# Kernel optimization log

Measured on AMD Instinct MI355X. Metric: run time of the kernel, lower is better.

## Reference

```python
import jax, jax.numpy as jnp
import numpy as np

B, L, T, H = 8, 16, 1024, 256


def setup_inputs() -> dict:
    key = jax.random.key(0)
    k1, k2 = jax.random.split(key)
    h_blth = jax.random.normal(k1, (B, L, T, H), dtype=jnp.float32)
    # nn.Linear(H, 1): weight [1, H] -> store as [H]; bias [1]
    attn_w = jax.random.normal(k2, (H,), dtype=jnp.float32) / np.sqrt(H)
    attn_b = jnp.zeros((1,), dtype=jnp.float32)
    return {"h_blth": h_blth, "attn_w": attn_w, "attn_b": attn_b}


def reference(h_blth, attn_w, attn_b):
    # scores: [B, L, T]
    s = jnp.einsum('blth,h->blt', h_blth, attn_w) + attn_b[0]
    # global max over T (matches torch .max(dim=2, keepdim=True))
    s_max = jnp.max(s, axis=2, keepdims=True)
    exp_s = jnp.exp(s - s_max)                      # [B, L, T]
    cum_exp = jnp.cumsum(exp_s, axis=2)             # [B, L, T]
    weighted_h = exp_s[..., None] * h_blth          # [B, L, T, H]
    cum_weighted_h = jnp.cumsum(weighted_h, axis=2) # [B, L, T, H]
    ctx = cum_weighted_h / (cum_exp[..., None] + 1e-12)
    return h_blth + ctx
```

## Files before the change

### kernel.cpp

```cpp
#include <hip/hip_runtime.h>


constexpr int Tn = 1024, Hn = 256;
constexpr int BL = 128;
constexpr int NCH = 8;
constexpr int CT = Tn / NCH;
constexpr int F4 = Hn / 4;

__global__ __launch_bounds__(256) void k_scores(const float* __restrict__ h,
                                                const float* __restrict__ w,
                                                const float* __restrict__ bias,
                                                float* __restrict__ ebuf,
                                                float* __restrict__ P,
                                                float* __restrict__ Se) {
    const int wave = threadIdx.x >> 6, lane = threadIdx.x & 63;
    const int g = lane >> 4, sub = lane & 15;
    const int j = blockIdx.x & 7, bl = blockIdx.x >> 3;
    const float b0 = bias[0];
    const float4* wp = reinterpret_cast<const float4*>(w);
    float4 w4[4];
    #pragma unroll
    for (int q = 0; q < 4; ++q) w4[q] = wp[sub + 16 * q];
    const float4* hp = reinterpret_cast<const float4*>(h) + (size_t)bl * Tn * F4;
    const int t0 = j * CT + wave * 32;

    float4 acc[4] = {{0,0,0,0},{0,0,0,0},{0,0,0,0},{0,0,0,0}};
    float esum = 0.f;
    #pragma unroll
    for (int i = 0; i < 8; ++i) {
        const int t = t0 + i * 4 + g;
        float4 x[4];
        #pragma unroll
        for (int q = 0; q < 4; ++q) x[q] = hp[(size_t)t * F4 + sub + 16 * q];
        float p = 0.f;
        #pragma unroll
        for (int q = 0; q < 4; ++q) {
            p = fmaf(x[q].x, w4[q].x, p);
            p = fmaf(x[q].y, w4[q].y, p);
            p = fmaf(x[q].z, w4[q].z, p);
            p = fmaf(x[q].w, w4[q].w, p);
        }
        p += __shfl_xor(p, 1, 64);
        p += __shfl_xor(p, 2, 64);
        p += __shfl_xor(p, 4, 64);
        p += __shfl_xor(p, 8, 64);
        const float e = __expf(p + b0);
        esum += e;
        #pragma unroll
        for (int q = 0; q < 4; ++q) {
            acc[q].x = fmaf(e, x[q].x, acc[q].x);
            acc[q].y = fmaf(e, x[q].y, acc[q].y);
            acc[q].z = fmaf(e, x[q].z, acc[q].z);
            acc[q].w = fmaf(e, x[q].w, acc[q].w);
        }
        if (sub == 0) ebuf[bl * Tn + t] = e;
    }
    #pragma unroll
    for (int q = 0; q < 4; ++q) {
        acc[q].x += __shfl_xor(acc[q].x, 16, 64); acc[q].x += __shfl_xor(acc[q].x, 32, 64);
        acc[q].y += __shfl_xor(acc[q].y, 16, 64); acc[q].y += __shfl_xor(acc[q].y, 32, 64);
        acc[q].z += __shfl_xor(acc[q].z, 16, 64); acc[q].z += __shfl_xor(acc[q].z, 32, 64);
        acc[q].w += __shfl_xor(acc[q].w, 16, 64); acc[q].w += __shfl_xor(acc[q].w, 32, 64);
    }
    esum += __shfl_xor(esum, 16, 64);  esum += __shfl_xor(esum, 32, 64);

    __shared__ float4 redP[4][16][4];
    __shared__ float  redS[4];
    if (lane < 16) {
        #pragma unroll
        for (int q = 0; q < 4; ++q) redP[wave][lane][q] = acc[q];
    }
    if (lane == 0) redS[wave] = esum;
    __syncthreads();
    if (threadIdx.x < 64) {
        const int s16 = threadIdx.x & 15, q = threadIdx.x >> 4;
        float4 a = redP[0][s16][q], b = redP[1][s16][q];
        float4 c = redP[2][s16][q], d = redP[3][s16][q];
        float4 s;
        s.x = (a.x + b.x) + (c.x + d.x);
        s.y = (a.y + b.y) + (c.y + d.y);
        s.z = (a.z + b.z) + (c.z + d.z);
        s.w = (a.w + b.w) + (c.w + d.w);
        reinterpret_cast<float4*>(P)[(bl * NCH + j) * F4 + s16 + 16 * q] = s;
    } else if (threadIdx.x == 64) {
        Se[bl * NCH + j] = (redS[0] + redS[1]) + (redS[2] + redS[3]);
    }
}

__global__ __launch_bounds__(256) void k_apply(const float* __restrict__ h,
                                               const float* __restrict__ ebuf,
                                               const float* __restrict__ P,
                                               const float* __restrict__ Se,
                                               float* __restrict__ out) {
    const int j = blockIdx.x & 7, bl = blockIdx.x >> 3;
    const int tid = threadIdx.x;
    __shared__ float se[CT], sd[CT];
    if (tid < CT) se[tid] = ebuf[bl * Tn + j * CT + tid];
    __syncthreads();

    if (tid < 64) {
        float base = 0.f;
        for (int jj = 0; jj < j; ++jj) base += Se[bl * NCH + jj];
        float v0 = se[2 * tid], v1 = se[2 * tid + 1];
        float ts = v0 + v1;
        float sc = ts;
        #pragma unroll
        for (int off = 1; off < 64; off <<= 1) {
            float n = __shfl_up(sc, off, 64);
            if (tid >= off) sc += n;
        }
        float pre = base + sc - ts;
        float c0 = pre + v0, c1 = c0 + v1;
        sd[2 * tid]     = 1.0f / (c0 + 1e-12f);
        sd[2 * tid + 1] = 1.0f / (c1 + 1e-12f);
    }
    float acc = 0.f;
    for (int jj = 0; jj < j; ++jj) acc += P[(bl * NCH + jj) * Hn + tid];
    __syncthreads();

    const float* hp = h   + ((size_t)bl * Tn + j * CT) * Hn + tid;
    float*       op = out + ((size_t)bl * Tn + j * CT) * Hn + tid;

    for (int t = 0; t < CT; t += 16) {
        float x[16];
        #pragma unroll
        for (int u = 0; u < 16; ++u) x[u] = hp[(size_t)(t + u) * Hn];
        #pragma unroll
        for (int u = 0; u < 16; ++u) {
            acc = fmaf(se[t + u], x[u], acc);
            op[(size_t)(t + u) * Hn] = fmaf(acc, sd[t + u], x[u]);
        }
    }
}

extern "C" void kernel_launch(void* const* d_in, const int* in_sizes, int n_in,
                              void* d_out, int out_size, void* d_ws, size_t ws_size,
                              hipStream_t stream) {
    const float* h = (const float*)d_in[0];
    const float* w = (const float*)d_in[1];
    const float* b = (const float*)d_in[2];
    float* out = (float*)d_out;

    float* ebuf = (float*)d_ws;
    float* P    = ebuf + BL * Tn;
    float* Se   = P + BL * NCH * Hn;

    k_scores<<<BL * NCH, 256, 0, stream>>>(h, w, b, ebuf, P, Se);
    k_apply<<<BL * NCH, 256, 0, stream>>>(h, ebuf, P, Se, out);
}
```

Before: 253.8 us.

## Fuse score and apply kernels with decoupled-lookback chunk prefix and LDS-cached rows

Replaces the two-kernel design, where h was read twice from global memory, with a single kernel. Each block gets a dynamic ticket, loads a 64-row chunk into LDS, computes scores, exps and the chunk partial sums, and publishes them with a release flag. It then spin-waits on the flags of earlier chunks to build its prefix offset and writes the output from the LDS copy. This roughly halves the HBM reads of h, at the cost of a memset per call, serialized waits on predecessor chunks, and 64KB of LDS per block, which limits occupancy.

```diff
diff --git a/kernel.cpp b/kernel.cpp
--- a/kernel.cpp
+++ b/kernel.cpp
@@ -2,134 +2,124 @@
 
 
 constexpr int Tn = 1024, Hn = 256;
-constexpr int BL = 128;
-constexpr int NCH = 8;
-constexpr int CT = Tn / NCH;
-constexpr int F4 = Hn / 4;
+constexpr int BL   = 128;
+constexpr int CT   = 64;
+constexpr int NCH  = Tn / CT;
+constexpr int F4   = Hn / 4;
+constexpr int NBLK = BL * NCH;
 
-__global__ __launch_bounds__(256) void k_scores(const float* __restrict__ h,
-                                                const float* __restrict__ w,
-                                                const float* __restrict__ bias,
-                                                float* __restrict__ ebuf,
-                                                float* __restrict__ P,
-                                                float* __restrict__ Se) {
-    const int wave = threadIdx.x >> 6, lane = threadIdx.x & 63;
-    const int g = lane >> 4, sub = lane & 15;
-    const int j = blockIdx.x & 7, bl = blockIdx.x >> 3;
-    const float b0 = bias[0];
-    const float4* wp = reinterpret_cast<const float4*>(w);
-    float4 w4[4];
-    #pragma unroll
-    for (int q = 0; q < 4; ++q) w4[q] = wp[sub + 16 * q];
-    const float4* hp = reinterpret_cast<const float4*>(h) + (size_t)bl * Tn * F4;
-    const int t0 = j * CT + wave * 32;
+__global__ __launch_bounds__(256) void k_fused(
+    const float* __restrict__ h, const float* __restrict__ w,
+    const float* __restrict__ bias, float* __restrict__ out,
+    int* __restrict__ ticket, int* __restrict__ flags,
+    float* __restrict__ P, float* __restrict__ Se)
+{
+    const int tid  = threadIdx.x;
+    const int wv   = tid >> 6;
+    const int lane = tid & 63;
 
-    float4 acc[4] = {{0,0,0,0},{0,0,0,0},{0,0,0,0},{0,0,0,0}};
-    float esum = 0.f;
-    #pragma unroll
-    for (int i = 0; i < 8; ++i) {
-        const int t = t0 + i * 4 + g;
-        float4 x[4];
-        #pragma unroll
-        for (int q = 0; q < 4; ++q) x[q] = hp[(size_t)t * F4 + sub + 16 * q];
-        float p = 0.f;
-        #pragma unroll
-        for (int q = 0; q < 4; ++q) {
-            p = fmaf(x[q].x, w4[q].x, p);
-            p = fmaf(x[q].y, w4[q].y, p);
-            p = fmaf(x[q].z, w4[q].z, p);
-            p = fmaf(x[q].w, w4[q].w, p);
-        }
-        p += __shfl_xor(p, 1, 64);
-        p += __shfl_xor(p, 2, 64);
-        p += __shfl_xor(p, 4, 64);
-        p += __shfl_xor(p, 8, 64);
+    __shared__ float4 hbuf[CT * F4];
+    __shared__ float  e_s[CT], cums[CT], sdv[CT];
+    __shared__ float4 PW[4][F4];
+    __shared__ float  esw[4];
+    __shared__ int    vb_s;
+
+    if (tid == 0) vb_s = atomicAdd(ticket, 1);
+    __syncthreads();
+    const int vbid = vb_s;
+    const int j  = vbid >> 7;
+    const int bl = vbid & (BL - 1);
+
+    const float  b0 = bias[0];
+    const float4 w4 = reinterpret_cast<const float4*>(w)[lane];
+    const float4* __restrict__ h4 = reinterpret_cast<const float4*>(h);
+    const size_t rowbase = ((size_t)bl * Tn + (size_t)j * CT) * F4;
+
+    float4 acc = make_float4(0.f, 0.f, 0.f, 0.f);
+    float  esum = 0.f;
+    const int r0 = wv * 16;
+    #pragma unroll 4
+    for (int i = 0; i < 16; ++i) {
+        const int r = r0 + i;
+        const float4 x = h4[rowbase + (size_t)r * F4 + lane];
+        float p = x.x * w4.x + x.y * w4.y + x.z * w4.z + x.w * w4.w;
+        p += __shfl_xor(p, 1);  p += __shfl_xor(p, 2);  p += __shfl_xor(p, 4);
+        p += __shfl_xor(p, 8);  p += __shfl_xor(p, 16); p += __shfl_xor(p, 32);
         const float e = __expf(p + b0);
         esum += e;
+        acc.x = fmaf(e, x.x, acc.x); acc.y = fmaf(e, x.y, acc.y);
+        acc.z = fmaf(e, x.z, acc.z); acc.w = fmaf(e, x.w, acc.w);
+        hbuf[r * F4 + lane] = x;
+        if (lane == 0) e_s[r] = e;
+    }
+    PW[wv][lane] = acc;
+    if (lane == 0) esw[wv] = esum;
+    __syncthreads();
+
+    if (wv == 0) {
+        float c = e_s[lane];
         #pragma unroll
-        for (int q = 0; q < 4; ++q) {
-            acc[q].x = fmaf(e, x[q].x, acc[q].x);
-            acc[q].y = fmaf(e, x[q].y, acc[q].y);
-            acc[q].z = fmaf(e, x[q].z, acc[q].z);
-            acc[q].w = fmaf(e, x[q].w, acc[q].w);
+        for (int off = 1; off < 64; off <<= 1) {
+            const float n = __shfl_up(c, off);
+            if (lane >= off) c += n;
         }
-        if (sub == 0) ebuf[bl * Tn + t] = e;
+        cums[lane] = c;
+    } else if (wv == 1) {
+        float4 p4 = PW[0][lane];
+        const float4 q1 = PW[1][lane], q2 = PW[2][lane], q3 = PW[3][lane];
+        p4.x += q1.x + q2.x + q3.x;  p4.y += q1.y + q2.y + q3.y;
+        p4.z += q1.z + q2.z + q3.z;  p4.w += q1.w + q2.w + q3.w;
+        reinterpret_cast<float4*>(P)[(size_t)vbid * F4 + lane] = p4;
+        if (lane == 0) Se[vbid] = (esw[0] + esw[1]) + (esw[2] + esw[3]);
+        __threadfence();
+        if (lane == 0)
+            __hip_atomic_store(&flags[vbid], 1, __ATOMIC_RELEASE,
+                               __HIP_MEMORY_SCOPE_AGENT);
+    }
+
+    float seo = 0.f;
+    if (lane < j) {
+        const int pf = lane * BL + bl;
+        while (__hip_atomic_load(&flags[pf], __ATOMIC_ACQUIRE,
+                                 __HIP_MEMORY_SCOPE_AGENT) == 0) {
+            __builtin_amdgcn_s_sleep(2);
+        }
+        seo = Se[pf];
+    }
+    seo += __shfl_xor(seo, 1); seo += __shfl_xor(seo, 2);
+    seo += __shfl_xor(seo, 4); seo += __shfl_xor(seo, 8);
+    seo = __shfl(seo, 0);
+
+    float4 off4 = make_float4(0.f, 0.f, 0.f, 0.f);
+    for (int jj = 0; jj < j; ++jj) {
+        const float4 q =
+            reinterpret_cast<const float4*>(P)[((size_t)jj * BL + bl) * F4 + lane];
+        off4.x += q.x; off4.y += q.y; off4.z += q.z; off4.w += q.w;
     }
     #pragma unroll
-    for (int q = 0; q < 4; ++q) {
-        acc[q].x += __shfl_xor(acc[q].x, 16, 64); acc[q].x += __shfl_xor(acc[q].x, 32, 64);
-        acc[q].y += __shfl_xor(acc[q].y, 16, 64); acc[q].y += __shfl_xor(acc[q].y, 32, 64);
-        acc[q].z += __shfl_xor(acc[q].z, 16, 64); acc[q].z += __shfl_xor(acc[q].z, 32, 64);
-        acc[q].w += __shfl_xor(acc[q].w, 16, 64); acc[q].w += __shfl_xor(acc[q].w, 32, 64);
+    for (int ww = 0; ww < 3; ++ww) {
+        if (ww < wv) {
+            const float4 q = PW[ww][lane];
+            off4.x += q.x; off4.y += q.y; off4.z += q.z; off4.w += q.w;
+        }
     }
-    esum += __shfl_xor(esum, 16, 64);  esum += __shfl_xor(esum, 32, 64);
-
-    __shared__ float4 redP[4][16][4];
-    __shared__ float  redS[4];
-    if (lane < 16) {
-        #pragma unroll
-        for (int q = 0; q < 4; ++q) redP[wave][lane][q] = acc[q];
-    }
-    if (lane == 0) redS[wave] = esum;
-    __syncthreads();
-    if (threadIdx.x < 64) {
-        const int s16 = threadIdx.x & 15, q = threadIdx.x >> 4;
-        float4 a = redP[0][s16][q], b = redP[1][s16][q];
-        float4 c = redP[2][s16][q], d = redP[3][s16][q];
-        float4 s;
-        s.x = (a.x + b.x) + (c.x + d.x);
-        s.y = (a.y + b.y) + (c.y + d.y);
-        s.z = (a.z + b.z) + (c.z + d.z);
-        s.w = (a.w + b.w) + (c.w + d.w);
-        reinterpret_cast<float4*>(P)[(bl * NCH + j) * F4 + s16 + 16 * q] = s;
-    } else if (threadIdx.x == 64) {
-        Se[bl * NCH + j] = (redS[0] + redS[1]) + (redS[2] + redS[3]);
-    }
-}
-
-__global__ __launch_bounds__(256) void k_apply(const float* __restrict__ h,
-                                               const float* __restrict__ ebuf,
-                                               const float* __restrict__ P,
-                                               const float* __restrict__ Se,
-                                               float* __restrict__ out) {
-    const int j = blockIdx.x & 7, bl = blockIdx.x >> 3;
-    const int tid = threadIdx.x;
-    __shared__ float se[CT], sd[CT];
-    if (tid < CT) se[tid] = ebuf[bl * Tn + j * CT + tid];
+    if (wv == 0) sdv[lane] = 1.0f / (seo + cums[lane] + 1e-12f);
     __syncthreads();
 
-    if (tid < 64) {
-        float base = 0.f;
-        for (int jj = 0; jj < j; ++jj) base += Se[bl * NCH + jj];
-        float v0 = se[2 * tid], v1 = se[2 * tid + 1];
-        float ts = v0 + v1;
-        float sc = ts;
-        #pragma unroll
-        for (int off = 1; off < 64; off <<= 1) {
-            float n = __shfl_up(sc, off, 64);
-            if (tid >= off) sc += n;
-        }
-        float pre = base + sc - ts;
-        float c0 = pre + v0, c1 = c0 + v1;
-        sd[2 * tid]     = 1.0f / (c0 + 1e-12f);
-        sd[2 * tid + 1] = 1.0f / (c1 + 1e-12f);
-    }
-    float acc = 0.f;
-    for (int jj = 0; jj < j; ++jj) acc += P[(bl * NCH + jj) * Hn + tid];
-    __syncthreads();
-
-    const float* hp = h   + ((size_t)bl * Tn + j * CT) * Hn + tid;
-    float*       op = out + ((size_t)bl * Tn + j * CT) * Hn + tid;
-
-    for (int t = 0; t < CT; t += 16) {
-        float x[16];
-        #pragma unroll
-        for (int u = 0; u < 16; ++u) x[u] = hp[(size_t)(t + u) * Hn];
-        #pragma unroll
-        for (int u = 0; u < 16; ++u) {
-            acc = fmaf(se[t + u], x[u], acc);
-            op[(size_t)(t + u) * Hn] = fmaf(acc, sd[t + u], x[u]);
-        }
+    float4 a = off4;
+    float4* __restrict__ o4 = reinterpret_cast<float4*>(out);
+    #pragma unroll
+    for (int u = 0; u < 16; ++u) {
+        const int r = r0 + u;
+        const float4 x = hbuf[r * F4 + lane];
+        const float  e = e_s[r];
+        a.x = fmaf(e, x.x, a.x); a.y = fmaf(e, x.y, a.y);
+        a.z = fmaf(e, x.z, a.z); a.w = fmaf(e, x.w, a.w);
+        const float s = sdv[r];
+        float4 o;
+        o.x = fmaf(a.x, s, x.x); o.y = fmaf(a.y, s, x.y);
+        o.z = fmaf(a.z, s, x.z); o.w = fmaf(a.w, s, x.w);
+        o4[rowbase + (size_t)r * F4 + lane] = o;
     }
 }
 
@@ -141,10 +131,12 @@
     const float* b = (const float*)d_in[2];
     float* out = (float*)d_out;
 
-    float* ebuf = (float*)d_ws;
-    float* P    = ebuf + BL * Tn;
-    float* Se   = P + BL * NCH * Hn;
+    char* ws = (char*)d_ws;
+    int*   ticket = (int*)ws;
+    int*   flags  = (int*)(ws + 64);
+    float* P      = (float*)(ws + 16384);
+    float* Se     = (float*)(ws + 16384 + (size_t)NBLK * Hn * 4);
 
-    k_scores<<<BL * NCH, 256, 0, stream>>>(h, w, b, ebuf, P, Se);
-    k_apply<<<BL * NCH, 256, 0, stream>>>(h, ebuf, P, Se, out);
+    hipMemsetAsync(d_ws, 0, 64 + NBLK * sizeof(int), stream);
+    k_fused<<<NBLK, 256, 0, stream>>>(h, w, b, out, ticket, flags, P, Se);
 }
```

Result: slower. 565.9 us (+122.9%).

## Split scan into per-wave 32-step segments with float4 lanes over H

Applied to the files above, without the earlier changes.

Partial sums of the scan are now stored per wave (32 timesteps) instead of per block (128 timesteps), so the per-block shared-memory reduction and its __syncthreads go away. In the apply kernel each wave handles its own 32-timestep segment with float4 lanes covering H. Running prefixes are broadcast through wave shuffles, so there are no shared-memory arrays or block barriers. The serial dependency chain per thread becomes 32 steps, at the cost of summing up to 31 prefix partials per wave and a larger workspace.

```diff
diff --git a/kernel.cpp b/kernel.cpp
--- a/kernel.cpp
+++ b/kernel.cpp
@@ -2,17 +2,18 @@
 
 
 constexpr int Tn = 1024, Hn = 256;
-constexpr int BL = 128;
+constexpr int BL  = 128;
 constexpr int NCH = 8;
-constexpr int CT = Tn / NCH;
-constexpr int F4 = Hn / 4;
+constexpr int CT  = Tn / NCH;
+constexpr int F4  = Hn / 4;
+constexpr int NW  = Tn / 32;
 
 __global__ __launch_bounds__(256) void k_scores(const float* __restrict__ h,
                                                 const float* __restrict__ w,
                                                 const float* __restrict__ bias,
                                                 float* __restrict__ ebuf,
-                                                float* __restrict__ P,
-                                                float* __restrict__ Se) {
+                                                float* __restrict__ P32,
+                                                float* __restrict__ Se32) {
     const int wave = threadIdx.x >> 6, lane = threadIdx.x & 63;
     const int g = lane >> 4, sub = lane & 15;
     const int j = blockIdx.x & 7, bl = blockIdx.x >> 3;
@@ -40,10 +41,10 @@
             p = fmaf(x[q].z, w4[q].z, p);
             p = fmaf(x[q].w, w4[q].w, p);
         }
-        p += __shfl_xor(p, 1, 64);
-        p += __shfl_xor(p, 2, 64);
-        p += __shfl_xor(p, 4, 64);
-        p += __shfl_xor(p, 8, 64);
+        p += __shfl_xor(p, 1);
+        p += __shfl_xor(p, 2);
+        p += __shfl_xor(p, 4);
+        p += __shfl_xor(p, 8);
         const float e = __expf(p + b0);
         esum += e;
         #pragma unroll
@@ -57,78 +58,78 @@
     }
     #pragma unroll
     for (int q = 0; q < 4; ++q) {
-        acc[q].x += __shfl_xor(acc[q].x, 16, 64); acc[q].x += __shfl_xor(acc[q].x, 32, 64);
-        acc[q].y += __shfl_xor(acc[q].y, 16, 64); acc[q].y += __shfl_xor(acc[q].y, 32, 64);
-        acc[q].z += __shfl_xor(acc[q].z, 16, 64); acc[q].z += __shfl_xor(acc[q].z, 32, 64);
-        acc[q].w += __shfl_xor(acc[q].w, 16, 64); acc[q].w += __shfl_xor(acc[q].w, 32, 64);
+        acc[q].x += __shfl_xor(acc[q].x, 16); acc[q].x += __shfl_xor(acc[q].x, 32);
+        acc[q].y += __shfl_xor(acc[q].y, 16); acc[q].y += __shfl_xor(acc[q].y, 32);
+        acc[q].z += __shfl_xor(acc[q].z, 16); acc[q].z += __shfl_xor(acc[q].z, 32);
+        acc[q].w += __shfl_xor(acc[q].w, 16); acc[q].w += __shfl_xor(acc[q].w, 32);
     }
-    esum += __shfl_xor(esum, 16, 64);  esum += __shfl_xor(esum, 32, 64);
+    esum += __shfl_xor(esum, 16);  esum += __shfl_xor(esum, 32);
 
-    __shared__ float4 redP[4][16][4];
-    __shared__ float  redS[4];
+    const int W = j * 4 + wave;
     if (lane < 16) {
-        #pragma unroll
-        for (int q = 0; q < 4; ++q) redP[wave][lane][q] = acc[q];
+        float4* pp = reinterpret_cast<float4*>(P32) + ((size_t)bl * NW + W) * F4;
+        pp[sub]      = acc[0];
+        pp[sub + 16] = acc[1];
+        pp[sub + 32] = acc[2];
+        pp[sub + 48] = acc[3];
     }
-    if (lane == 0) redS[wave] = esum;
-    __syncthreads();
-    if (threadIdx.x < 64) {
-        const int s16 = threadIdx.x & 15, q = threadIdx.x >> 4;
-        float4 a = redP[0][s16][q], b = redP[1][s16][q];
-        float4 c = redP[2][s16][q], d = redP[3][s16][q];
-        float4 s;
-        s.x = (a.x + b.x) + (c.x + d.x);
-        s.y = (a.y + b.y) + (c.y + d.y);
-        s.z = (a.z + b.z) + (c.z + d.z);
-        s.w = (a.w + b.w) + (c.w + d.w);
-        reinterpret_cast<float4*>(P)[(bl * NCH + j) * F4 + s16 + 16 * q] = s;
-    } else if (threadIdx.x == 64) {
-        Se[bl * NCH + j] = (redS[0] + redS[1]) + (redS[2] + redS[3]);
-    }
+    if (lane == 0) Se32[bl * NW + W] = esum;
 }
 
 __global__ __launch_bounds__(256) void k_apply(const float* __restrict__ h,
                                                const float* __restrict__ ebuf,
-                                               const float* __restrict__ P,
-                                               const float* __restrict__ Se,
+                                               const float* __restrict__ P32,
+                                               const float* __restrict__ Se32,
                                                float* __restrict__ out) {
+    const int wave = threadIdx.x >> 6, lane = threadIdx.x & 63;
     const int j = blockIdx.x & 7, bl = blockIdx.x >> 3;
-    const int tid = threadIdx.x;
-    __shared__ float se[CT], sd[CT];
-    if (tid < CT) se[tid] = ebuf[bl * Tn + j * CT + tid];
-    __syncthreads();
+    const int W = j * 4 + wave;
+    const int t0 = W * 32;
 
-    if (tid < 64) {
-        float base = 0.f;
-        for (int jj = 0; jj < j; ++jj) base += Se[bl * NCH + jj];
-        float v0 = se[2 * tid], v1 = se[2 * tid + 1];
-        float ts = v0 + v1;
-        float sc = ts;
+    const float4* Pp = reinterpret_cast<const float4*>(P32) + (size_t)bl * NW * F4;
+    float4 off4 = make_float4(0.f, 0.f, 0.f, 0.f);
+    for (int q = 0; q < W; ++q) {
+        const float4 v = Pp[q * F4 + lane];
+        off4.x += v.x; off4.y += v.y; off4.z += v.z; off4.w += v.w;
+    }
+    float seo = 0.f;
+    if (lane < W) seo = Se32[bl * NW + lane];
+    seo += __shfl_xor(seo, 1); seo += __shfl_xor(seo, 2);
+    seo += __shfl_xor(seo, 4); seo += __shfl_xor(seo, 8);
+    seo += __shfl_xor(seo, 16);
+    seo = __shfl(seo, 0);
+
+    float ev = 0.f;
+    if (lane < 32) ev = ebuf[bl * Tn + t0 + lane];
+    float sc = ev;
+    #pragma unroll
+    for (int off = 1; off < 32; off <<= 1) {
+        const float n = __shfl_up(sc, off);
+        if (lane >= off) sc += n;
+    }
+    const float sdv = 1.0f / (seo + sc + 1e-12f);
+
+    const float4* hp = reinterpret_cast<const float4*>(h)
+                       + ((size_t)bl * Tn + t0) * F4 + lane;
+    float4* op = reinterpret_cast<float4*>(out)
+                 + ((size_t)bl * Tn + t0) * F4 + lane;
+
+    float4 a = off4;
+    #pragma unroll
+    for (int i = 0; i < 32; i += 8) {
+        float4 x[8];
         #pragma unroll
-        for (int off = 1; off < 64; off <<= 1) {
-            float n = __shfl_up(sc, off, 64);
-            if (tid >= off) sc += n;
-        }
-        float pre = base + sc - ts;
-        float c0 = pre + v0, c1 = c0 + v1;
-        sd[2 * tid]     = 1.0f / (c0 + 1e-12f);
-        sd[2 * tid + 1] = 1.0f / (c1 + 1e-12f);
-    }
-    float acc = 0.f;
-    for (int jj = 0; jj < j; ++jj) acc += P[(bl * NCH + jj) * Hn + tid];
-    __syncthreads();
-
-    const float* hp = h   + ((size_t)bl * Tn + j * CT) * Hn + tid;
-    float*       op = out + ((size_t)bl * Tn + j * CT) * Hn + tid;
-
-    for (int t = 0; t < CT; t += 16) {
-        float x[16];
+        for (int u = 0; u < 8; ++u) x[u] = hp[(size_t)(i + u) * F4];
         #pragma unroll
-        for (int u = 0; u < 16; ++u) x[u] = hp[(size_t)(t + u) * Hn];
-        #pragma unroll
-        for (int u = 0; u < 16; ++u) {
-            acc = fmaf(se[t + u], x[u], acc);
-            op[(size_t)(t + u) * Hn] = fmaf(acc, sd[t + u], x[u]);
+        for (int u = 0; u < 8; ++u) {
+            const float e = __shfl(ev,  i + u);
+            const float s = __shfl(sdv, i + u);
+            a.x = fmaf(e, x[u].x, a.x); a.y = fmaf(e, x[u].y, a.y);
+            a.z = fmaf(e, x[u].z, a.z); a.w = fmaf(e, x[u].w, a.w);
+            float4 o;
+            o.x = fmaf(a.x, s, x[u].x); o.y = fmaf(a.y, s, x[u].y);
+            o.z = fmaf(a.z, s, x[u].z); o.w = fmaf(a.w, s, x[u].w);
+            op[(size_t)(i + u) * F4] = o;
         }
     }
 }
@@ -142,9 +143,9 @@
     float* out = (float*)d_out;
 
     float* ebuf = (float*)d_ws;
-    float* P    = ebuf + BL * Tn;
-    float* Se   = P + BL * NCH * Hn;
+    float* P32  = ebuf + BL * Tn;
+    float* Se32 = P32 + (size_t)BL * NW * Hn;
 
-    k_scores<<<BL * NCH, 256, 0, stream>>>(h, w, b, ebuf, P, Se);
-    k_apply<<<BL * NCH, 256, 0, stream>>>(h, ebuf, P, Se, out);
+    k_scores<<<BL * NCH, 256, 0, stream>>>(h, w, b, ebuf, P32, Se32);
+    k_apply <<<BL * NCH, 256, 0, stream>>>(h, ebuf, P32, Se32, out);
 }
```

New measurement: 262.0 us. 1.03x slower.
